# Kernel tuning notes

Hardware: AMD Instinct MI355X
Metric: run time of the kernel (lower is better)

Reference implementation:

```python
import jax, jax.numpy as jnp
import numpy as np

N, IN_DIM, LAT, K = 32768, 128, 64, 8192
BETA = 1.25


def _linear_params(key, d_in, d_out):
    kw, kb = jax.random.split(key)
    lim = 1.0 / np.sqrt(d_in)
    W = jax.random.uniform(kw, (d_out, d_in), minval=-lim, maxval=lim, dtype=jnp.float32)
    b = jax.random.uniform(kb, (d_out,), minval=-lim, maxval=lim, dtype=jnp.float32)
    return W, b


def setup_inputs() -> dict:
    key = jax.random.key(0)
    ks = jax.random.split(key, 9)
    x = jax.random.normal(ks[0], (N, IN_DIM), dtype=jnp.float32)
    # encoder: 128 -> 256 -> 128 -> 64
    enc_W1, enc_b1 = _linear_params(ks[1], IN_DIM, 256)
    enc_W2, enc_b2 = _linear_params(ks[2], 256, 128)
    enc_W3, enc_b3 = _linear_params(ks[3], 128, LAT)
    # codebook: uniform(-1/K, 1/K)
    emb = jax.random.uniform(ks[4], (K, LAT), minval=-1.0 / K, maxval=1.0 / K, dtype=jnp.float32)
    # decoder: 64 -> 128 -> 256 -> (mu: 128, log_var: 128)
    dec_W1, dec_b1 = _linear_params(ks[5], LAT, 128)
    dec_W2, dec_b2 = _linear_params(ks[6], 128, 256)
    dec_Wmu, dec_bmu = _linear_params(ks[7], 256, IN_DIM)
    dec_Wlv, dec_blv = _linear_params(ks[8], 256, IN_DIM)
    return {
        'x': x,
        'enc_W1': enc_W1, 'enc_b1': enc_b1,
        'enc_W2': enc_W2, 'enc_b2': enc_b2,
        'enc_W3': enc_W3, 'enc_b3': enc_b3,
        'emb': emb,
        'dec_W1': dec_W1, 'dec_b1': dec_b1,
        'dec_W2': dec_W2, 'dec_b2': dec_b2,
        'dec_Wmu': dec_Wmu, 'dec_bmu': dec_bmu,
        'dec_Wlv': dec_Wlv, 'dec_blv': dec_blv,
    }


def reference(x, enc_W1, enc_b1, enc_W2, enc_b2, enc_W3, enc_b3, emb,
              dec_W1, dec_b1, dec_W2, dec_b2, dec_Wmu, dec_bmu, dec_Wlv, dec_blv):
    sg = jax.lax.stop_gradient
    # encoder MLP
    h = jax.nn.relu(x @ enc_W1.T + enc_b1)
    h = jax.nn.relu(h @ enc_W2.T + enc_b2)
    lat = h @ enc_W3.T + enc_b3                      # [N, D]
    # vector quantizer: [N, K] pairwise squared distances
    d = (jnp.sum(lat * lat, axis=1, keepdims=True)
         + jnp.sum(emb * emb, axis=1)
         - 2.0 * lat @ emb.T)
    inds = jnp.argmin(d, axis=1)                     # [N]
    one_hot = jax.nn.one_hot(inds, K, dtype=jnp.float32)   # [N, K]
    q = emb[inds]                                    # gather == one_hot @ emb
    commitment = jnp.mean((sg(q) - lat) ** 2)
    embedding_loss = jnp.mean((q - sg(lat)) ** 2)
    vq_loss = BETA * commitment + embedding_loss
    z = lat + sg(q - lat)                            # straight-through
    # decoder MLP
    h = jax.nn.relu(z @ dec_W1.T + dec_b1)
    h = jax.nn.relu(h @ dec_W2.T + dec_b2)
    x_hat = h @ dec_Wmu.T + dec_bmu
    x_hat_var = h @ dec_Wlv.T + dec_blv
    return x_hat, x_hat_var, one_hot, vq_loss
```

## Files before the change

### kernel.cpp

```cpp
#include <hip/hip_runtime.h>
#include <cfloat>
#include <climits>

#define TPB 256


__global__ __launch_bounds__(TPB) void wt_kernel(
    const float* __restrict__ W1, const float* __restrict__ W2,
    const float* __restrict__ W3, const float* __restrict__ U1,
    const float* __restrict__ U2, const float* __restrict__ Umu,
    const float* __restrict__ Ulv, float* __restrict__ wt) {
  __shared__ float sB[64 * 68];
  const int b = blockIdx.x;
  const float* src; int R, C, lt; float* dst;
  if (b < 8)       { src = W1;  R = 256; C = 128; dst = wt;          lt = b; }
  else if (b < 16) { src = W2;  R = 128; C = 256; dst = wt + 32768;  lt = b - 8; }
  else if (b < 18) { src = W3;  R = 64;  C = 128; dst = wt + 65536;  lt = b - 16; }
  else if (b < 20) { src = U1;  R = 128; C = 64;  dst = wt + 73728;  lt = b - 18; }
  else if (b < 28) { src = U2;  R = 256; C = 128; dst = wt + 81920;  lt = b - 20; }
  else if (b < 36) { src = Umu; R = 128; C = 256; dst = wt + 114688; lt = b - 28; }
  else             { src = Ulv; R = 128; C = 256; dst = wt + 147456; lt = b - 36; }
  const int tiles_r = R >> 6;
  const int r0 = (lt % tiles_r) << 6, c0 = (lt / tiles_r) << 6;
  const int t = threadIdx.x;
  for (int v = t; v < 1024; v += TPB) {
    const int c4 = v & 15, r = v >> 4;
    const float4 w =
        *reinterpret_cast<const float4*>(src + (size_t)(r0 + r) * C + c0 + 4 * c4);
    *reinterpret_cast<float4*>(&sB[r * 68 + 4 * c4]) = w;
  }
  __syncthreads();
  for (int v = t; v < 1024; v += TPB) {
    const int r4 = v & 15, c = v >> 4;
    float4 o;
    o.x = sB[(4 * r4 + 0) * 68 + c];
    o.y = sB[(4 * r4 + 1) * 68 + c];
    o.z = sB[(4 * r4 + 2) * 68 + c];
    o.w = sB[(4 * r4 + 3) * 68 + c];
    *reinterpret_cast<float4*>(dst + (size_t)(c0 + c) * R + r0 + 4 * r4) = o;
  }
}

__global__ __launch_bounds__(TPB) void embt_kernel(const float* __restrict__ emb,
                                                   float* __restrict__ embT,
                                                   float* __restrict__ En) {
  __shared__ float sB[64 * 68];
  const int c0 = blockIdx.x * 64;
  const int t = threadIdx.x;
  for (int v = t; v < 1024; v += TPB) {
    const int d4 = v & 15, r = v >> 4;
    const float4 e =
        *reinterpret_cast<const float4*>(emb + (size_t)(c0 + r) * 64 + 4 * d4);
    *reinterpret_cast<float4*>(&sB[r * 68 + 4 * d4]) = e;
  }
  __syncthreads();
  if (t < 64) {
    const float* row = &sB[t * 68];
    float q[8];
#pragma unroll
    for (int j = 0; j < 8; ++j) q[j] = __fmul_rn(row[j], row[j]);
#pragma unroll
    for (int m = 1; m < 8; ++m)
#pragma unroll
      for (int j = 0; j < 8; ++j) {
        const float v = row[m * 8 + j];
        q[j] = __fadd_rn(q[j], __fmul_rn(v, v));
      }
    En[c0 + t] = __fadd_rn(
        __fadd_rn(__fadd_rn(q[0], q[1]), __fadd_rn(q[2], q[3])),
        __fadd_rn(__fadd_rn(q[4], q[5]), __fadd_rn(q[6], q[7])));
  }
  for (int v = t; v < 1024; v += TPB) {
    const int r4 = v & 15, d = v >> 4;
    float4 o;
    o.x = sB[(4 * r4 + 0) * 68 + d];
    o.y = sB[(4 * r4 + 1) * 68 + d];
    o.z = sB[(4 * r4 + 2) * 68 + d];
    o.w = sB[(4 * r4 + 3) * 68 + d];
    *reinterpret_cast<float4*>(embT + (size_t)d * 8192 + c0 + 4 * r4) = o;
  }
}

__global__ __launch_bounds__(512) void enc_fused(
    const float* __restrict__ x, const float* __restrict__ WT1,
    const float* __restrict__ WT2, const float* __restrict__ WT3,
    const float* __restrict__ b1, const float* __restrict__ b2,
    const float* __restrict__ b3, float* __restrict__ lat) {
  __shared__ float sX[128 * 68];
  __shared__ float sH1[256 * 68];
  __shared__ float sH2[128 * 68];
  const int t = threadIdx.x;
  const int m0 = blockIdx.x * 64;

  for (int v = t; v < 2048; v += 512) {
    const int k4 = v & 31, r = v >> 5;
    const float4 xv =
        *reinterpret_cast<const float4*>(x + (size_t)(m0 + r) * 128 + 4 * k4);
    float* dst = &sX[(4 * k4) * 68 + r];
    dst[0] = xv.x; dst[68] = xv.y; dst[136] = xv.z; dst[204] = xv.w;
  }
  __syncthreads();

  {
    const int cg8 = (t & 31) * 8, rg4 = (t >> 5) * 4;
    float acc[4][8] = {};
#pragma unroll 8
    for (int k = 0; k < 128; ++k) {
      const float4 a = *reinterpret_cast<const float4*>(&sX[k * 68 + rg4]);
      const float* wr = WT1 + (size_t)k * 256 + cg8;
      const float4 b0 = *reinterpret_cast<const float4*>(wr);
      const float4 b1v = *reinterpret_cast<const float4*>(wr + 4);
      const float av[4] = {a.x, a.y, a.z, a.w};
      const float bv[8] = {b0.x, b0.y, b0.z, b0.w, b1v.x, b1v.y, b1v.z, b1v.w};
#pragma unroll
      for (int i = 0; i < 4; ++i)
#pragma unroll
        for (int j = 0; j < 8; ++j) acc[i][j] = fmaf(av[i], bv[j], acc[i][j]);
    }
#pragma unroll
    for (int j = 0; j < 8; ++j) {
      const int col = cg8 + j;
      const float bj = b1[col];
#pragma unroll
      for (int i = 0; i < 4; ++i) {
        const float h = __fadd_rn(acc[i][j], bj);
        sH1[col * 68 + rg4 + i] = h > 0.f ? h : 0.f;
      }
    }
  }
  __syncthreads();

  {
    const int cg4 = (t & 31) * 4, rg4 = (t >> 5) * 4;
    float acc[4][4] = {};
#pragma unroll 8
    for (int k = 0; k < 256; ++k) {
      const float4 a = *reinterpret_cast<const float4*>(&sH1[k * 68 + rg4]);
      const float4 bb =
          *reinterpret_cast<const float4*>(WT2 + (size_t)k * 128 + cg4);
      const float av[4] = {a.x, a.y, a.z, a.w};
      const float bv[4] = {bb.x, bb.y, bb.z, bb.w};
#pragma unroll
      for (int i = 0; i < 4; ++i)
#pragma unroll
        for (int j = 0; j < 4; ++j) acc[i][j] = fmaf(av[i], bv[j], acc[i][j]);
    }
#pragma unroll
    for (int j = 0; j < 4; ++j) {
      const int col = cg4 + j;
      const float bj = b2[col];
#pragma unroll
      for (int i = 0; i < 4; ++i) {
        const float h = __fadd_rn(acc[i][j], bj);
        sH2[col * 68 + rg4 + i] = h > 0.f ? h : 0.f;
      }
    }
  }
  __syncthreads();

  {
    const int cg4 = (t & 15) * 4, rg2 = (t >> 4) * 2;
    float acc[2][4] = {};
#pragma unroll 8
    for (int k = 0; k < 128; ++k) {
      const float2 a = *reinterpret_cast<const float2*>(&sH2[k * 68 + rg2]);
      const float4 bb =
          *reinterpret_cast<const float4*>(WT3 + (size_t)k * 64 + cg4);
      const float av[2] = {a.x, a.y};
      const float bv[4] = {bb.x, bb.y, bb.z, bb.w};
#pragma unroll
      for (int i = 0; i < 2; ++i)
#pragma unroll
        for (int j = 0; j < 4; ++j) acc[i][j] = fmaf(av[i], bv[j], acc[i][j]);
    }
#pragma unroll
    for (int i = 0; i < 2; ++i) {
      float4 o;
      o.x = __fadd_rn(acc[i][0], b3[cg4 + 0]);
      o.y = __fadd_rn(acc[i][1], b3[cg4 + 1]);
      o.z = __fadd_rn(acc[i][2], b3[cg4 + 2]);
      o.w = __fadd_rn(acc[i][3], b3[cg4 + 3]);
      *reinterpret_cast<float4*>(lat + (size_t)(m0 + rg2 + i) * 64 + cg4) = o;
    }
  }
}

__global__ __launch_bounds__(512, 6) void vq_kernel(
    const float* __restrict__ lat, const float* __restrict__ embT,
    const float* __restrict__ En, int* __restrict__ inds,
    float* __restrict__ lossp, float* __restrict__ oh) {
  __shared__ float sL[64 * 68];
  __shared__ float sE[64 * 132];
  __shared__ float sEn[128];
  __shared__ float snl[64];
  __shared__ int ridx[64];
  __shared__ float lacc;
  const int t = threadIdx.x;
  const int tx = t & 31, ty = t >> 5;
  const int r0 = ty * 4;
  const int tx4 = tx * 4;
  const int m0 = blockIdx.x * 64;

  for (int v = t; v < 1024; v += 512) {
    const int r = v >> 4, d4 = v & 15;
    const float4 lv =
        *reinterpret_cast<const float4*>(lat + (size_t)(m0 + r) * 64 + 4 * d4);
    float* dst = &sL[(4 * d4) * 68 + r];
    dst[0] = lv.x; dst[68] = lv.y; dst[136] = lv.z; dst[204] = lv.w;
  }
  if (t == 0) lacc = 0.f;
  __syncthreads();
  if (t < 64) {
    float q[8];
#pragma unroll
    for (int j = 0; j < 8; ++j) {
      const float v = sL[j * 68 + t];
      q[j] = __fmul_rn(v, v);
    }
#pragma unroll
    for (int m = 1; m < 8; ++m)
#pragma unroll
      for (int j = 0; j < 8; ++j) {
        const float v = sL[(m * 8 + j) * 68 + t];
        q[j] = __fadd_rn(q[j], __fmul_rn(v, v));
      }
    snl[t] = __fadd_rn(
        __fadd_rn(__fadd_rn(q[0], q[1]), __fadd_rn(q[2], q[3])),
        __fadd_rn(__fadd_rn(q[4], q[5]), __fadd_rn(q[6], q[7])));
  }
  __syncthreads();
  float nl[4];
#pragma unroll
  for (int i = 0; i < 4; ++i) nl[i] = snl[r0 + i];

  float v1[4];
  int i1[4];
#pragma unroll
  for (int i = 0; i < 4; ++i) { v1[i] = FLT_MAX; i1[i] = INT_MAX; }

  for (int ch = 0; ch < 64; ++ch) {
    const int c0 = ch * 128;
    __syncthreads();
    for (int v = t; v < 2048; v += 512) {
      const int cl = v & 31, d = v >> 5;
      const float4 e = *reinterpret_cast<const float4*>(
          embT + (size_t)d * 8192 + c0 + 4 * cl);
      *reinterpret_cast<float4*>(&sE[d * 132 + 4 * cl]) = e;
    }
    if (t < 128) sEn[t] = En[c0 + t];
    __syncthreads();

    float acc[4][4] = {};
#pragma unroll 4
    for (int d = 0; d < 64; ++d) {
      const float4 a = *reinterpret_cast<const float4*>(&sL[d * 68 + r0]);
      const float4 bb = *reinterpret_cast<const float4*>(&sE[d * 132 + tx4]);
      const float av[4] = {a.x, a.y, a.z, a.w};
      const float bv[4] = {bb.x, bb.y, bb.z, bb.w};
#pragma unroll
      for (int i = 0; i < 4; ++i)
#pragma unroll
        for (int j = 0; j < 4; ++j) acc[i][j] = fmaf(av[i], bv[j], acc[i][j]);
    }
#pragma unroll
    for (int j = 0; j < 4; ++j) {
      const float Ec = sEn[tx4 + j];
      const int c = c0 + tx4 + j;
#pragma unroll
      for (int i = 0; i < 4; ++i) {
        const float t1 = __fadd_rn(nl[i], Ec);
        const float s = __fsub_rn(t1, __fmul_rn(2.0f, acc[i][j]));
        if (s < v1[i]) { v1[i] = s; i1[i] = c; }
      }
    }
    const float4 z = make_float4(0.f, 0.f, 0.f, 0.f);
    for (int v = t; v < 2048; v += 512) {
      const int r = v >> 5, c4 = v & 31;
      *reinterpret_cast<float4*>(oh + (size_t)(m0 + r) * 8192 + c0 + 4 * c4) =
          z;
    }
  }

#pragma unroll
  for (int m = 16; m >= 1; m >>= 1) {
#pragma unroll
    for (int i = 0; i < 4; ++i) {
      const float ov = __shfl_xor(v1[i], m);
      const int oi = __shfl_xor(i1[i], m);
      if (ov < v1[i] || (ov == v1[i] && oi < i1[i])) {
        v1[i] = ov; i1[i] = oi;
      }
    }
  }
  if (tx == 0) {
    float ls = 0.f;
#pragma unroll
    for (int i = 0; i < 4; ++i) {
      ridx[r0 + i] = i1[i];
      inds[m0 + r0 + i] = i1[i];
      ls += v1[i];
    }
    atomicAdd(&lacc, ls);
  }
  __syncthreads();
  if (t == 0) lossp[blockIdx.x] = lacc;

  for (int v = t; v < 2048; v += 512) {
    const int r = v >> 5, c4 = v & 31;
    const int ind = ridx[r];
    const int g4 = ind >> 2;
    if ((g4 & 31) == c4) {
      float4 o = make_float4(0.f, 0.f, 0.f, 0.f);
      reinterpret_cast<float*>(&o)[ind & 3] = 1.f;
      *reinterpret_cast<float4*>(oh + (size_t)(m0 + r) * 8192 + 4 * g4) = o;
    }
  }
}

__global__ __launch_bounds__(512) void dec_fused(
    const float* __restrict__ emb, const int* __restrict__ inds,
    const float* __restrict__ WT1, const float* __restrict__ b1,
    const float* __restrict__ WT2, const float* __restrict__ b2,
    const float* __restrict__ WTmu, const float* __restrict__ bmu,
    const float* __restrict__ WTlv, const float* __restrict__ blv,
    float* __restrict__ xh, float* __restrict__ xv) {
  __shared__ float sQ[64 * 68];
  __shared__ float sG1[128 * 68];
  __shared__ float sG2[256 * 68];
  const int t = threadIdx.x;
  const int m0 = blockIdx.x * 64;

  for (int v = t; v < 1024; v += 512) {
    const int k4 = v & 15, r = v >> 4;
    const int id = inds[m0 + r];
    const float4 e =
        *reinterpret_cast<const float4*>(emb + (size_t)id * 64 + 4 * k4);
    float* dst = &sQ[(4 * k4) * 68 + r];
    dst[0] = e.x; dst[68] = e.y; dst[136] = e.z; dst[204] = e.w;
  }
  __syncthreads();

  {
    const int cg4 = (t & 31) * 4, rg4 = (t >> 5) * 4;
    float acc[4][4] = {};
#pragma unroll 8
    for (int k = 0; k < 64; ++k) {
      const float4 a = *reinterpret_cast<const float4*>(&sQ[k * 68 + rg4]);
      const float4 bb =
          *reinterpret_cast<const float4*>(WT1 + (size_t)k * 128 + cg4);
      const float av[4] = {a.x, a.y, a.z, a.w};
      const float bv[4] = {bb.x, bb.y, bb.z, bb.w};
#pragma unroll
      for (int i = 0; i < 4; ++i)
#pragma unroll
        for (int j = 0; j < 4; ++j) acc[i][j] = fmaf(av[i], bv[j], acc[i][j]);
    }
#pragma unroll
    for (int j = 0; j < 4; ++j) {
      const int col = cg4 + j;
      const float bj = b1[col];
#pragma unroll
      for (int i = 0; i < 4; ++i) {
        const float h = acc[i][j] + bj;
        sG1[col * 68 + rg4 + i] = h > 0.f ? h : 0.f;
      }
    }
  }
  __syncthreads();

  {
    const int cg8 = (t & 31) * 8, rg4 = (t >> 5) * 4;
    float acc[4][8] = {};
#pragma unroll 8
    for (int k = 0; k < 128; ++k) {
      const float4 a = *reinterpret_cast<const float4*>(&sG1[k * 68 + rg4]);
      const float* wr = WT2 + (size_t)k * 256 + cg8;
      const float4 b0 = *reinterpret_cast<const float4*>(wr);
      const float4 b1v = *reinterpret_cast<const float4*>(wr + 4);
      const float av[4] = {a.x, a.y, a.z, a.w};
      const float bv[8] = {b0.x, b0.y, b0.z, b0.w, b1v.x, b1v.y, b1v.z, b1v.w};
#pragma unroll
      for (int i = 0; i < 4; ++i)
#pragma unroll
        for (int j = 0; j < 8; ++j) acc[i][j] = fmaf(av[i], bv[j], acc[i][j]);
    }
#pragma unroll
    for (int j = 0; j < 8; ++j) {
      const int col = cg8 + j;
      const float bj = b2[col];
#pragma unroll
      for (int i = 0; i < 4; ++i) {
        const float h = acc[i][j] + bj;
        sG2[col * 68 + rg4 + i] = h > 0.f ? h : 0.f;
      }
    }
  }
  __syncthreads();

  for (int head = 0; head < 2; ++head) {
    const float* WT = head ? WTlv : WTmu;
    const float* bb_ = head ? blv : bmu;
    float* o = head ? xv : xh;
    const int cg4 = (t & 31) * 4, rg4 = (t >> 5) * 4;
    float acc[4][4] = {};
#pragma unroll 8
    for (int k = 0; k < 256; ++k) {
      const float4 a = *reinterpret_cast<const float4*>(&sG2[k * 68 + rg4]);
      const float4 bb =
          *reinterpret_cast<const float4*>(WT + (size_t)k * 128 + cg4);
      const float av[4] = {a.x, a.y, a.z, a.w};
      const float bv[4] = {bb.x, bb.y, bb.z, bb.w};
#pragma unroll
      for (int i = 0; i < 4; ++i)
#pragma unroll
        for (int j = 0; j < 4; ++j) acc[i][j] = fmaf(av[i], bv[j], acc[i][j]);
    }
#pragma unroll
    for (int i = 0; i < 4; ++i) {
      float4 ov;
      ov.x = acc[i][0] + bb_[cg4 + 0];
      ov.y = acc[i][1] + bb_[cg4 + 1];
      ov.z = acc[i][2] + bb_[cg4 + 2];
      ov.w = acc[i][3] + bb_[cg4 + 3];
      *reinterpret_cast<float4*>(o + (size_t)(m0 + rg4 + i) * 128 + cg4) = ov;
    }
  }
}

__global__ void fin_kernel(const float* __restrict__ lossp,
                           float* __restrict__ outp) {
  const int t = threadIdx.x;
  double s = 0.0;
  for (int i = t; i < 512; i += 64) s += (double)lossp[i];
#pragma unroll
  for (int m = 32; m >= 1; m >>= 1) s += __shfl_xor(s, m);
  if (t == 0) *outp = (float)(2.25 * s / (32768.0 * 64.0));
}

extern "C" void kernel_launch(void* const* d_in, const int* in_sizes, int n_in,
                              void* d_out, int out_size, void* d_ws,
                              size_t ws_size, hipStream_t stream) {
  const float* x = (const float*)d_in[0];
  const float* eW1 = (const float*)d_in[1];
  const float* eb1 = (const float*)d_in[2];
  const float* eW2 = (const float*)d_in[3];
  const float* eb2 = (const float*)d_in[4];
  const float* eW3 = (const float*)d_in[5];
  const float* eb3 = (const float*)d_in[6];
  const float* emb = (const float*)d_in[7];
  const float* dW1 = (const float*)d_in[8];
  const float* db1 = (const float*)d_in[9];
  const float* dW2 = (const float*)d_in[10];
  const float* db2 = (const float*)d_in[11];
  const float* dWmu = (const float*)d_in[12];
  const float* dbmu = (const float*)d_in[13];
  const float* dWlv = (const float*)d_in[14];
  const float* dblv = (const float*)d_in[15];

  float* out = (float*)d_out;
  float* xhat = out;
  float* xvar = out + 4194304;
  float* oh = out + 8388608;
  float* lossout = out + 276824064;

  float* lat = (float*)d_ws;
  float* En = lat + 2097152;
  float* lossp = En + 8192;
  int* inds = (int*)(lossp + 512);
  float* embT = (float*)(inds + 32768);
  float* wt = embT + 524288;
  float* wt1 = wt;
  float* wt2 = wt + 32768;
  float* wt3 = wt + 65536;
  float* uwt1 = wt + 73728;
  float* uwt2 = wt + 81920;
  float* uwtmu = wt + 114688;
  float* uwtlv = wt + 147456;

  wt_kernel<<<44, TPB, 0, stream>>>(eW1, eW2, eW3, dW1, dW2, dWmu, dWlv, wt);
  embt_kernel<<<128, TPB, 0, stream>>>(emb, embT, En);
  enc_fused<<<512, 512, 0, stream>>>(x, wt1, wt2, wt3, eb1, eb2, eb3, lat);
  vq_kernel<<<512, 512, 0, stream>>>(lat, embT, En, inds, lossp, oh);
  dec_fused<<<512, 512, 0, stream>>>(emb, inds, uwt1, db1, uwt2, db2, uwtmu,
                                     dbmu, uwtlv, dblv, xhat, xvar);
  fin_kernel<<<1, 64, 0, stream>>>(lossp, lossout);
}
```

Measured before the change: 824.7 us.

## Enlarge VQ distance tile to 128x256 with 8x8 register blocking and prefetch

The VQ kernel now handles 128 rows per block against 256-code chunks, and each thread computes an 8x8 accumulator tile instead of 4x4. This raises arithmetic intensity per shared-memory load and halves the number of code-chunk iterations. The next codebook chunk is prefetched into registers while the current one is being computed, then written to LDS between barriers. The grid halves to 256 blocks and occupancy drops (launch bounds 512,2), with larger LDS use and register pressure. On a 256-CU part this may leave some CUs idle.

New measurement: 834.5 us. Within noise of the previous version (+1.2%).

```diff
diff --git a/kernel.cpp b/kernel.cpp
--- a/kernel.cpp
+++ b/kernel.cpp
@@ -185,43 +185,48 @@
   }
 }
 
-__global__ __launch_bounds__(512, 6) void vq_kernel(
+__global__ __launch_bounds__(512, 2) void vq_kernel(
     const float* __restrict__ lat, const float* __restrict__ embT,
     const float* __restrict__ En, int* __restrict__ inds,
     float* __restrict__ lossp, float* __restrict__ oh) {
-  __shared__ float sL[64 * 68];
-  __shared__ float sE[64 * 132];
-  __shared__ float sEn[128];
-  __shared__ float snl[64];
-  __shared__ int ridx[64];
+  __shared__ float sL[64 * 132];
+  __shared__ float sE[64 * 260];
+  __shared__ float snl[128];
+  __shared__ int ridx[128];
   __shared__ float lacc;
   const int t = threadIdx.x;
-  const int tx = t & 31, ty = t >> 5;
-  const int r0 = ty * 4;
-  const int tx4 = tx * 4;
-  const int m0 = blockIdx.x * 64;
-
-  for (int v = t; v < 1024; v += 512) {
+  const int cg = t & 31;
+  const int rg = t >> 5;
+  const int cg4 = cg * 4;
+  const int rg4 = rg * 4;
+  const int m0 = blockIdx.x * 128;
+
+  for (int v = t; v < 2048; v += 512) {
     const int r = v >> 4, d4 = v & 15;
     const float4 lv =
         *reinterpret_cast<const float4*>(lat + (size_t)(m0 + r) * 64 + 4 * d4);
-    float* dst = &sL[(4 * d4) * 68 + r];
-    dst[0] = lv.x; dst[68] = lv.y; dst[136] = lv.z; dst[204] = lv.w;
+    float* dst = &sL[(4 * d4) * 132 + r];
+    dst[0] = lv.x; dst[132] = lv.y; dst[264] = lv.z; dst[396] = lv.w;
+  }
+  for (int v = t; v < 4096; v += 512) {
+    const int d = v >> 6, c4 = v & 63;
+    *reinterpret_cast<float4*>(&sE[d * 260 + 4 * c4]) =
+        *reinterpret_cast<const float4*>(embT + (size_t)d * 8192 + 4 * c4);
   }
   if (t == 0) lacc = 0.f;
   __syncthreads();
-  if (t < 64) {
+  if (t < 128) {
     float q[8];
 #pragma unroll
     for (int j = 0; j < 8; ++j) {
-      const float v = sL[j * 68 + t];
+      const float v = sL[j * 132 + t];
       q[j] = __fmul_rn(v, v);
     }
 #pragma unroll
     for (int m = 1; m < 8; ++m)
 #pragma unroll
       for (int j = 0; j < 8; ++j) {
-        const float v = sL[(m * 8 + j) * 68 + t];
+        const float v = sL[(m * 8 + j) * 132 + t];
         q[j] = __fadd_rn(q[j], __fmul_rn(v, v));
       }
     snl[t] = __fadd_rn(
@@ -229,62 +234,87 @@
         __fadd_rn(__fadd_rn(q[4], q[5]), __fadd_rn(q[6], q[7])));
   }
   __syncthreads();
-  float nl[4];
-#pragma unroll
-  for (int i = 0; i < 4; ++i) nl[i] = snl[r0 + i];
-
-  float v1[4];
-  int i1[4];
-#pragma unroll
-  for (int i = 0; i < 4; ++i) { v1[i] = FLT_MAX; i1[i] = INT_MAX; }
-
-  for (int ch = 0; ch < 64; ++ch) {
-    const int c0 = ch * 128;
-    __syncthreads();
-    for (int v = t; v < 2048; v += 512) {
-      const int cl = v & 31, d = v >> 5;
-      const float4 e = *reinterpret_cast<const float4*>(
-          embT + (size_t)d * 8192 + c0 + 4 * cl);
-      *reinterpret_cast<float4*>(&sE[d * 132 + 4 * cl]) = e;
-    }
-    if (t < 128) sEn[t] = En[c0 + t];
-    __syncthreads();
-
-    float acc[4][4] = {};
-#pragma unroll 4
+  float nl[8];
+#pragma unroll
+  for (int i = 0; i < 4; ++i) {
+    nl[i] = snl[rg4 + i];
+    nl[4 + i] = snl[64 + rg4 + i];
+  }
+
+  float v1[8];
+  int i1[8];
+#pragma unroll
+  for (int i = 0; i < 8; ++i) { v1[i] = FLT_MAX; i1[i] = INT_MAX; }
+
+  const float4 z = make_float4(0.f, 0.f, 0.f, 0.f);
+
+  for (int ch = 0; ch < 32; ++ch) {
+    const int c0 = ch << 8;
+    float4 pf[8];
+    if (ch < 31) {
+      const int cn = c0 + 256;
+#pragma unroll
+      for (int k = 0; k < 8; ++k) {
+        const int v = t + (k << 9);
+        const int d = v >> 6, c4 = v & 63;
+        pf[k] = *reinterpret_cast<const float4*>(embT + (size_t)d * 8192 +
+                                                 cn + 4 * c4);
+      }
+    }
+    const float4 EA = *reinterpret_cast<const float4*>(En + c0 + cg4);
+    const float4 EB = *reinterpret_cast<const float4*>(En + c0 + 128 + cg4);
+
+    float acc[8][8] = {};
+#pragma unroll 2
     for (int d = 0; d < 64; ++d) {
-      const float4 a = *reinterpret_cast<const float4*>(&sL[d * 68 + r0]);
-      const float4 bb = *reinterpret_cast<const float4*>(&sE[d * 132 + tx4]);
-      const float av[4] = {a.x, a.y, a.z, a.w};
-      const float bv[4] = {bb.x, bb.y, bb.z, bb.w};
-#pragma unroll
-      for (int i = 0; i < 4; ++i)
-#pragma unroll
-        for (int j = 0; j < 4; ++j) acc[i][j] = fmaf(av[i], bv[j], acc[i][j]);
-    }
-#pragma unroll
-    for (int j = 0; j < 4; ++j) {
-      const float Ec = sEn[tx4 + j];
-      const int c = c0 + tx4 + j;
-#pragma unroll
-      for (int i = 0; i < 4; ++i) {
+      const float4 a0 = *reinterpret_cast<const float4*>(&sL[d * 132 + rg4]);
+      const float4 a1 =
+          *reinterpret_cast<const float4*>(&sL[d * 132 + 64 + rg4]);
+      const float4 b0 = *reinterpret_cast<const float4*>(&sE[d * 260 + cg4]);
+      const float4 b1 =
+          *reinterpret_cast<const float4*>(&sE[d * 260 + 128 + cg4]);
+      const float av[8] = {a0.x, a0.y, a0.z, a0.w, a1.x, a1.y, a1.z, a1.w};
+      const float bv[8] = {b0.x, b0.y, b0.z, b0.w, b1.x, b1.y, b1.z, b1.w};
+#pragma unroll
+      for (int i = 0; i < 8; ++i)
+#pragma unroll
+        for (int j = 0; j < 8; ++j) acc[i][j] = fmaf(av[i], bv[j], acc[i][j]);
+    }
+    const float Ev[8] = {EA.x, EA.y, EA.z, EA.w, EB.x, EB.y, EB.z, EB.w};
+#pragma unroll
+    for (int j = 0; j < 8; ++j) {
+      const int c = c0 + (j < 4 ? cg4 + j : 128 + cg4 + (j - 4));
+      const float Ec = Ev[j];
+#pragma unroll
+      for (int i = 0; i < 8; ++i) {
         const float t1 = __fadd_rn(nl[i], Ec);
         const float s = __fsub_rn(t1, __fmul_rn(2.0f, acc[i][j]));
         if (s < v1[i]) { v1[i] = s; i1[i] = c; }
       }
     }
-    const float4 z = make_float4(0.f, 0.f, 0.f, 0.f);
-    for (int v = t; v < 2048; v += 512) {
-      const int r = v >> 5, c4 = v & 31;
+#pragma unroll
+    for (int k = 0; k < 16; ++k) {
+      const int v = t + (k << 9);
+      const int r = v >> 6, c4 = v & 63;
       *reinterpret_cast<float4*>(oh + (size_t)(m0 + r) * 8192 + c0 + 4 * c4) =
           z;
     }
+    __syncthreads();
+    if (ch < 31) {
+#pragma unroll
+      for (int k = 0; k < 8; ++k) {
+        const int v = t + (k << 9);
+        const int d = v >> 6, c4 = v & 63;
+        *reinterpret_cast<float4*>(&sE[d * 260 + 4 * c4]) = pf[k];
+      }
+    }
+    __syncthreads();
   }
 
 #pragma unroll
   for (int m = 16; m >= 1; m >>= 1) {
 #pragma unroll
-    for (int i = 0; i < 4; ++i) {
+    for (int i = 0; i < 8; ++i) {
       const float ov = __shfl_xor(v1[i], m);
       const int oi = __shfl_xor(i1[i], m);
       if (ov < v1[i] || (ov == v1[i] && oi < i1[i])) {
@@ -292,24 +322,29 @@
       }
     }
   }
-  if (tx == 0) {
+  if (cg == 0) {
     float ls = 0.f;
 #pragma unroll
     for (int i = 0; i < 4; ++i) {
-      ridx[r0 + i] = i1[i];
-      inds[m0 + r0 + i] = i1[i];
+      ridx[rg4 + i] = i1[i];
+      inds[m0 + rg4 + i] = i1[i];
       ls += v1[i];
+      ridx[64 + rg4 + i] = i1[4 + i];
+      inds[m0 + 64 + rg4 + i] = i1[4 + i];
+      ls += v1[4 + i];
     }
     atomicAdd(&lacc, ls);
   }
   __syncthreads();
   if (t == 0) lossp[blockIdx.x] = lacc;
 
-  for (int v = t; v < 2048; v += 512) {
-    const int r = v >> 5, c4 = v & 31;
+#pragma unroll
+  for (int k = 0; k < 16; ++k) {
+    const int v = t + (k << 9);
+    const int r = v >> 6, c4 = v & 63;
     const int ind = ridx[r];
     const int g4 = ind >> 2;
-    if ((g4 & 31) == c4) {
+    if ((g4 & 63) == c4) {
       float4 o = make_float4(0.f, 0.f, 0.f, 0.f);
       reinterpret_cast<float*>(&o)[ind & 3] = 1.f;
       *reinterpret_cast<float4*>(oh + (size_t)(m0 + r) * 8192 + 4 * g4) = o;
@@ -431,7 +466,7 @@
                            float* __restrict__ outp) {
   const int t = threadIdx.x;
   double s = 0.0;
-  for (int i = t; i < 512; i += 64) s += (double)lossp[i];
+  for (int i = t; i < 256; i += 64) s += (double)lossp[i];
 #pragma unroll
   for (int m = 32; m >= 1; m >>= 1) s += __shfl_xor(s, m);
   if (t == 0) *outp = (float)(2.25 * s / (32768.0 * 64.0));
@@ -480,7 +515,7 @@
   wt_kernel<<<44, TPB, 0, stream>>>(eW1, eW2, eW3, dW1, dW2, dWmu, dWlv, wt);
   embt_kernel<<<128, TPB, 0, stream>>>(emb, embT, En);
   enc_fused<<<512, 512, 0, stream>>>(x, wt1, wt2, wt3, eb1, eb2, eb3, lat);
-  vq_kernel<<<512, 512, 0, stream>>>(lat, embT, En, inds, lossp, oh);
+  vq_kernel<<<256, 512, 0, stream>>>(lat, embT, En, inds, lossp, oh);
   dec_fused<<<512, 512, 0, stream>>>(emb, inds, uwt1, db1, uwt2, db2, uwtmu,
                                      dbmu, uwtlv, dblv, xhat, xvar);
   fin_kernel<<<1, 64, 0, stream>>>(lossp, lossout);
```

## Fuse VQ search and decoder into one kernel with prefetch and nontemporal stores

Applied to the files above, without the earlier changes.

Merges the vector-quantizer kernel and the decoder MLP into a single kernel, so the chosen indices stay in shared memory and the separate inds global round trip and one launch go away. The codebook chunk for the next iteration is prefetched into registers while the current chunk is processed. The large one-hot zero fill and the decoder outputs now use nontemporal stores. The decoder's 256-wide hidden layer is split into two 128-column halves so one shared buffer can be reused, which cuts shared memory, and the occupancy hint is lowered from 6 to 4 blocks.

New measurement: 833.0 us. About the same (+1.0%).

```diff
diff --git a/kernel.cpp b/kernel.cpp
--- a/kernel.cpp
+++ b/kernel.cpp
@@ -4,6 +4,14 @@
 
 #define TPB 256
 
+
+typedef float f32x4 __attribute__((ext_vector_type(4)));
+
+__device__ __forceinline__ void nt_store4(float* p, float4 v) {
+  f32x4 nv;
+  nv.x = v.x; nv.y = v.y; nv.z = v.z; nv.w = v.w;
+  __builtin_nontemporal_store(nv, reinterpret_cast<f32x4*>(p));
+}
 
 __global__ __launch_bounds__(TPB) void wt_kernel(
     const float* __restrict__ W1, const float* __restrict__ W2,
@@ -185,244 +193,308 @@
   }
 }
 
-__global__ __launch_bounds__(512, 6) void vq_kernel(
+__global__ __launch_bounds__(512, 4) void vqdec_kernel(
     const float* __restrict__ lat, const float* __restrict__ embT,
-    const float* __restrict__ En, int* __restrict__ inds,
-    float* __restrict__ lossp, float* __restrict__ oh) {
-  __shared__ float sL[64 * 68];
-  __shared__ float sE[64 * 132];
-  __shared__ float sEn[128];
+    const float* __restrict__ En, const float* __restrict__ emb,
+    const float* __restrict__ UT1, const float* __restrict__ ub1,
+    const float* __restrict__ UT2, const float* __restrict__ ub2,
+    const float* __restrict__ UTmu, const float* __restrict__ ubmu,
+    const float* __restrict__ UTlv, const float* __restrict__ ublv,
+    float* __restrict__ oh, float* __restrict__ xh, float* __restrict__ xv,
+    float* __restrict__ lossp) {
+  __shared__ float smem[13056];
   __shared__ float snl[64];
   __shared__ int ridx[64];
   __shared__ float lacc;
   const int t = threadIdx.x;
-  const int tx = t & 31, ty = t >> 5;
-  const int r0 = ty * 4;
-  const int tx4 = tx * 4;
   const int m0 = blockIdx.x * 64;
 
-  for (int v = t; v < 1024; v += 512) {
-    const int r = v >> 4, d4 = v & 15;
-    const float4 lv =
-        *reinterpret_cast<const float4*>(lat + (size_t)(m0 + r) * 64 + 4 * d4);
-    float* dst = &sL[(4 * d4) * 68 + r];
-    dst[0] = lv.x; dst[68] = lv.y; dst[136] = lv.z; dst[204] = lv.w;
-  }
-  if (t == 0) lacc = 0.f;
-  __syncthreads();
-  if (t < 64) {
-    float q[8];
-#pragma unroll
-    for (int j = 0; j < 8; ++j) {
-      const float v = sL[j * 68 + t];
-      q[j] = __fmul_rn(v, v);
-    }
-#pragma unroll
-    for (int m = 1; m < 8; ++m)
+  {
+    float* const sL = smem;
+    float* const sE = smem + 4352;
+    const int cg = t & 31, rg = t >> 5;
+    const int cg4 = cg * 4, rg4 = rg * 4;
+
+    for (int v = t; v < 1024; v += 512) {
+      const int r = v >> 4, d4 = v & 15;
+      const float4 lv =
+          *reinterpret_cast<const float4*>(lat + (size_t)(m0 + r) * 64 + 4 * d4);
+      float* dst = &sL[(4 * d4) * 68 + r];
+      dst[0] = lv.x; dst[68] = lv.y; dst[136] = lv.z; dst[204] = lv.w;
+    }
+    if (t == 0) lacc = 0.f;
+    float4 st[4];
+#pragma unroll
+    for (int k = 0; k < 4; ++k) {
+      const int v = t + (k << 9);
+      const int d = v >> 5, c4 = v & 31;
+      st[k] = *reinterpret_cast<const float4*>(embT + (size_t)d * 8192 + 4 * c4);
+    }
+    __syncthreads();
+    if (t < 64) {
+      float q[8];
 #pragma unroll
       for (int j = 0; j < 8; ++j) {
-        const float v = sL[(m * 8 + j) * 68 + t];
-        q[j] = __fadd_rn(q[j], __fmul_rn(v, v));
-      }
-    snl[t] = __fadd_rn(
-        __fadd_rn(__fadd_rn(q[0], q[1]), __fadd_rn(q[2], q[3])),
-        __fadd_rn(__fadd_rn(q[4], q[5]), __fadd_rn(q[6], q[7])));
-  }
-  __syncthreads();
-  float nl[4];
-#pragma unroll
-  for (int i = 0; i < 4; ++i) nl[i] = snl[r0 + i];
-
-  float v1[4];
-  int i1[4];
-#pragma unroll
-  for (int i = 0; i < 4; ++i) { v1[i] = FLT_MAX; i1[i] = INT_MAX; }
-
-  for (int ch = 0; ch < 64; ++ch) {
-    const int c0 = ch * 128;
-    __syncthreads();
-    for (int v = t; v < 2048; v += 512) {
-      const int cl = v & 31, d = v >> 5;
-      const float4 e = *reinterpret_cast<const float4*>(
-          embT + (size_t)d * 8192 + c0 + 4 * cl);
-      *reinterpret_cast<float4*>(&sE[d * 132 + 4 * cl]) = e;
-    }
-    if (t < 128) sEn[t] = En[c0 + t];
-    __syncthreads();
-
-    float acc[4][4] = {};
+        const float v = sL[j * 68 + t];
+        q[j] = __fmul_rn(v, v);
+      }
+#pragma unroll
+      for (int m = 1; m < 8; ++m)
+#pragma unroll
+        for (int j = 0; j < 8; ++j) {
+          const float v = sL[(m * 8 + j) * 68 + t];
+          q[j] = __fadd_rn(q[j], __fmul_rn(v, v));
+        }
+      snl[t] = __fadd_rn(
+          __fadd_rn(__fadd_rn(q[0], q[1]), __fadd_rn(q[2], q[3])),
+          __fadd_rn(__fadd_rn(q[4], q[5]), __fadd_rn(q[6], q[7])));
+    }
+    __syncthreads();
+    float nl[4];
+#pragma unroll
+    for (int i = 0; i < 4; ++i) nl[i] = snl[rg4 + i];
+
+    float v1[4];
+    int i1[4];
+#pragma unroll
+    for (int i = 0; i < 4; ++i) { v1[i] = FLT_MAX; i1[i] = INT_MAX; }
+
+    const float4 z = make_float4(0.f, 0.f, 0.f, 0.f);
+
+    for (int ch = 0; ch < 64; ++ch) {
+      const int c0 = ch << 7;
+#pragma unroll
+      for (int k = 0; k < 4; ++k) {
+        const int v = t + (k << 9);
+        const int d = v >> 5, c4 = v & 31;
+        *reinterpret_cast<float4*>(&sE[d * 132 + 4 * c4]) = st[k];
+      }
+      __syncthreads();
+#pragma unroll
+      for (int k = 0; k < 4; ++k) {
+        const int v = t + (k << 9);
+        const int r = v >> 5, c4 = v & 31;
+        nt_store4(oh + (size_t)(m0 + r) * 8192 + c0 + 4 * c4, z);
+      }
+      if (ch < 63) {
+        const int cn = c0 + 128;
+#pragma unroll
+        for (int k = 0; k < 4; ++k) {
+          const int v = t + (k << 9);
+          const int d = v >> 5, c4 = v & 31;
+          st[k] = *reinterpret_cast<const float4*>(embT + (size_t)d * 8192 +
+                                                   cn + 4 * c4);
+        }
+      }
+      const float4 EA = *reinterpret_cast<const float4*>(En + c0 + cg4);
+
+      float acc[4][4] = {};
 #pragma unroll 4
-    for (int d = 0; d < 64; ++d) {
-      const float4 a = *reinterpret_cast<const float4*>(&sL[d * 68 + r0]);
-      const float4 bb = *reinterpret_cast<const float4*>(&sE[d * 132 + tx4]);
+      for (int d = 0; d < 64; ++d) {
+        const float4 a = *reinterpret_cast<const float4*>(&sL[d * 68 + rg4]);
+        const float4 bb = *reinterpret_cast<const float4*>(&sE[d * 132 + cg4]);
+        const float av[4] = {a.x, a.y, a.z, a.w};
+        const float bv[4] = {bb.x, bb.y, bb.z, bb.w};
+#pragma unroll
+        for (int i = 0; i < 4; ++i)
+#pragma unroll
+          for (int j = 0; j < 4; ++j) acc[i][j] = fmaf(av[i], bv[j], acc[i][j]);
+      }
+      const float Ev[4] = {EA.x, EA.y, EA.z, EA.w};
+#pragma unroll
+      for (int j = 0; j < 4; ++j) {
+        const int c = c0 + cg4 + j;
+        const float Ec = Ev[j];
+#pragma unroll
+        for (int i = 0; i < 4; ++i) {
+          const float t1 = __fadd_rn(nl[i], Ec);
+          const float s = __fsub_rn(t1, __fmul_rn(2.0f, acc[i][j]));
+          if (s < v1[i]) { v1[i] = s; i1[i] = c; }
+        }
+      }
+      __syncthreads();
+    }
+
+#pragma unroll
+    for (int m = 16; m >= 1; m >>= 1) {
+#pragma unroll
+      for (int i = 0; i < 4; ++i) {
+        const float ov = __shfl_xor(v1[i], m);
+        const int oi = __shfl_xor(i1[i], m);
+        if (ov < v1[i] || (ov == v1[i] && oi < i1[i])) {
+          v1[i] = ov; i1[i] = oi;
+        }
+      }
+    }
+    if (cg == 0) {
+      float ls = 0.f;
+#pragma unroll
+      for (int i = 0; i < 4; ++i) {
+        ridx[rg4 + i] = i1[i];
+        ls += v1[i];
+      }
+      atomicAdd(&lacc, ls);
+    }
+    __syncthreads();
+    if (t == 0) lossp[blockIdx.x] = lacc;
+
+#pragma unroll
+    for (int k = 0; k < 4; ++k) {
+      const int v = t + (k << 9);
+      const int r = v >> 5, c4 = v & 31;
+      const int ind = ridx[r];
+      const int g4 = ind >> 2;
+      if ((g4 & 31) == c4) {
+        float4 o = make_float4(0.f, 0.f, 0.f, 0.f);
+        reinterpret_cast<float*>(&o)[ind & 3] = 1.f;
+        nt_store4(oh + (size_t)(m0 + r) * 8192 + 4 * g4, o);
+      }
+    }
+  }
+
+  {
+    float* const sQ = smem;
+    float* const sG1 = smem + 4352;
+    float* const sG2 = smem;
+
+    for (int v = t; v < 1024; v += 512) {
+      const int k4 = v & 15, r = v >> 4;
+      const int id = ridx[r];
+      const float4 e =
+          *reinterpret_cast<const float4*>(emb + (size_t)id * 64 + 4 * k4);
+      float* dst = &sQ[(4 * k4) * 68 + r];
+      dst[0] = e.x; dst[68] = e.y; dst[136] = e.z; dst[204] = e.w;
+    }
+    __syncthreads();
+
+    const int cg4 = (t & 31) * 4, rg4 = (t >> 5) * 4;
+
+    {
+      float acc[4][4] = {};
+#pragma unroll 8
+      for (int k = 0; k < 64; ++k) {
+        const float4 a = *reinterpret_cast<const float4*>(&sQ[k * 68 + rg4]);
+        const float4 bb =
+            *reinterpret_cast<const float4*>(UT1 + (size_t)k * 128 + cg4);
+        const float av[4] = {a.x, a.y, a.z, a.w};
+        const float bv[4] = {bb.x, bb.y, bb.z, bb.w};
+#pragma unroll
+        for (int i = 0; i < 4; ++i)
+#pragma unroll
+          for (int j = 0; j < 4; ++j) acc[i][j] = fmaf(av[i], bv[j], acc[i][j]);
+      }
+#pragma unroll
+      for (int j = 0; j < 4; ++j) {
+        const int col = cg4 + j;
+        const float bj = ub1[col];
+#pragma unroll
+        for (int i = 0; i < 4; ++i) {
+          const float h = acc[i][j] + bj;
+          sG1[col * 68 + rg4 + i] = h > 0.f ? h : 0.f;
+        }
+      }
+    }
+    __syncthreads();
+
+    float accA[4][4] = {}, accB[4][4] = {};
+#pragma unroll 8
+    for (int k = 0; k < 128; ++k) {
+      const float4 a = *reinterpret_cast<const float4*>(&sG1[k * 68 + rg4]);
+      const float4 bA =
+          *reinterpret_cast<const float4*>(UT2 + (size_t)k * 256 + cg4);
+      const float4 bB =
+          *reinterpret_cast<const float4*>(UT2 + (size_t)k * 256 + 128 + cg4);
       const float av[4] = {a.x, a.y, a.z, a.w};
-      const float bv[4] = {bb.x, bb.y, bb.z, bb.w};
+      const float bAv[4] = {bA.x, bA.y, bA.z, bA.w};
+      const float bBv[4] = {bB.x, bB.y, bB.z, bB.w};
 #pragma unroll
       for (int i = 0; i < 4; ++i)
 #pragma unroll
-        for (int j = 0; j < 4; ++j) acc[i][j] = fmaf(av[i], bv[j], acc[i][j]);
-    }
-#pragma unroll
-    for (int j = 0; j < 4; ++j) {
-      const float Ec = sEn[tx4 + j];
-      const int c = c0 + tx4 + j;
-#pragma unroll
-      for (int i = 0; i < 4; ++i) {
-        const float t1 = __fadd_rn(nl[i], Ec);
-        const float s = __fsub_rn(t1, __fmul_rn(2.0f, acc[i][j]));
-        if (s < v1[i]) { v1[i] = s; i1[i] = c; }
-      }
-    }
-    const float4 z = make_float4(0.f, 0.f, 0.f, 0.f);
-    for (int v = t; v < 2048; v += 512) {
-      const int r = v >> 5, c4 = v & 31;
-      *reinterpret_cast<float4*>(oh + (size_t)(m0 + r) * 8192 + c0 + 4 * c4) =
-          z;
-    }
-  }
-
-#pragma unroll
-  for (int m = 16; m >= 1; m >>= 1) {
-#pragma unroll
-    for (int i = 0; i < 4; ++i) {
-      const float ov = __shfl_xor(v1[i], m);
-      const int oi = __shfl_xor(i1[i], m);
-      if (ov < v1[i] || (ov == v1[i] && oi < i1[i])) {
-        v1[i] = ov; i1[i] = oi;
-      }
-    }
-  }
-  if (tx == 0) {
-    float ls = 0.f;
-#pragma unroll
-    for (int i = 0; i < 4; ++i) {
-      ridx[r0 + i] = i1[i];
-      inds[m0 + r0 + i] = i1[i];
-      ls += v1[i];
-    }
-    atomicAdd(&lacc, ls);
-  }
-  __syncthreads();
-  if (t == 0) lossp[blockIdx.x] = lacc;
-
-  for (int v = t; v < 2048; v += 512) {
-    const int r = v >> 5, c4 = v & 31;
-    const int ind = ridx[r];
-    const int g4 = ind >> 2;
-    if ((g4 & 31) == c4) {
-      float4 o = make_float4(0.f, 0.f, 0.f, 0.f);
-      reinterpret_cast<float*>(&o)[ind & 3] = 1.f;
-      *reinterpret_cast<float4*>(oh + (size_t)(m0 + r) * 8192 + 4 * g4) = o;
-    }
-  }
-}
-
-__global__ __launch_bounds__(512) void dec_fused(
-    const float* __restrict__ emb, const int* __restrict__ inds,
-    const float* __restrict__ WT1, const float* __restrict__ b1,
-    const float* __restrict__ WT2, const float* __restrict__ b2,
-    const float* __restrict__ WTmu, const float* __restrict__ bmu,
-    const float* __restrict__ WTlv, const float* __restrict__ blv,
-    float* __restrict__ xh, float* __restrict__ xv) {
-  __shared__ float sQ[64 * 68];
-  __shared__ float sG1[128 * 68];
-  __shared__ float sG2[256 * 68];
-  const int t = threadIdx.x;
-  const int m0 = blockIdx.x * 64;
-
-  for (int v = t; v < 1024; v += 512) {
-    const int k4 = v & 15, r = v >> 4;
-    const int id = inds[m0 + r];
-    const float4 e =
-        *reinterpret_cast<const float4*>(emb + (size_t)id * 64 + 4 * k4);
-    float* dst = &sQ[(4 * k4) * 68 + r];
-    dst[0] = e.x; dst[68] = e.y; dst[136] = e.z; dst[204] = e.w;
-  }
-  __syncthreads();
-
-  {
-    const int cg4 = (t & 31) * 4, rg4 = (t >> 5) * 4;
-    float acc[4][4] = {};
-#pragma unroll 8
-    for (int k = 0; k < 64; ++k) {
-      const float4 a = *reinterpret_cast<const float4*>(&sQ[k * 68 + rg4]);
-      const float4 bb =
-          *reinterpret_cast<const float4*>(WT1 + (size_t)k * 128 + cg4);
-      const float av[4] = {a.x, a.y, a.z, a.w};
-      const float bv[4] = {bb.x, bb.y, bb.z, bb.w};
-#pragma unroll
-      for (int i = 0; i < 4; ++i)
-#pragma unroll
-        for (int j = 0; j < 4; ++j) acc[i][j] = fmaf(av[i], bv[j], acc[i][j]);
-    }
+        for (int j = 0; j < 4; ++j) {
+          accA[i][j] = fmaf(av[i], bAv[j], accA[i][j]);
+          accB[i][j] = fmaf(av[i], bBv[j], accB[i][j]);
+        }
+    }
+    __syncthreads();
+
 #pragma unroll
     for (int j = 0; j < 4; ++j) {
       const int col = cg4 + j;
-      const float bj = b1[col];
+      const float bj = ub2[col];
 #pragma unroll
       for (int i = 0; i < 4; ++i) {
-        const float h = acc[i][j] + bj;
-        sG1[col * 68 + rg4 + i] = h > 0.f ? h : 0.f;
-      }
-    }
-  }
-  __syncthreads();
-
-  {
-    const int cg8 = (t & 31) * 8, rg4 = (t >> 5) * 4;
-    float acc[4][8] = {};
-#pragma unroll 8
-    for (int k = 0; k < 128; ++k) {
-      const float4 a = *reinterpret_cast<const float4*>(&sG1[k * 68 + rg4]);
-      const float* wr = WT2 + (size_t)k * 256 + cg8;
-      const float4 b0 = *reinterpret_cast<const float4*>(wr);
-      const float4 b1v = *reinterpret_cast<const float4*>(wr + 4);
+        const float h = accA[i][j] + bj;
+        sG2[col * 68 + rg4 + i] = h > 0.f ? h : 0.f;
+      }
+    }
+    __syncthreads();
+
+    float accH[2][4][4] = {};
+#pragma unroll 8
+    for (int c = 0; c < 128; ++c) {
+      const float4 a = *reinterpret_cast<const float4*>(&sG2[c * 68 + rg4]);
+      const float4 bm =
+          *reinterpret_cast<const float4*>(UTmu + (size_t)c * 128 + cg4);
+      const float4 bl =
+          *reinterpret_cast<const float4*>(UTlv + (size_t)c * 128 + cg4);
       const float av[4] = {a.x, a.y, a.z, a.w};
-      const float bv[8] = {b0.x, b0.y, b0.z, b0.w, b1v.x, b1v.y, b1v.z, b1v.w};
+      const float bmv[4] = {bm.x, bm.y, bm.z, bm.w};
+      const float blv_[4] = {bl.x, bl.y, bl.z, bl.w};
 #pragma unroll
       for (int i = 0; i < 4; ++i)
 #pragma unroll
-        for (int j = 0; j < 8; ++j) acc[i][j] = fmaf(av[i], bv[j], acc[i][j]);
-    }
-#pragma unroll
-    for (int j = 0; j < 8; ++j) {
-      const int col = cg8 + j;
-      const float bj = b2[col];
+        for (int j = 0; j < 4; ++j) {
+          accH[0][i][j] = fmaf(av[i], bmv[j], accH[0][i][j]);
+          accH[1][i][j] = fmaf(av[i], blv_[j], accH[1][i][j]);
+        }
+    }
+    __syncthreads();
+
+#pragma unroll
+    for (int j = 0; j < 4; ++j) {
+      const int col = 128 + cg4 + j;
+      const float bj = ub2[col];
 #pragma unroll
       for (int i = 0; i < 4; ++i) {
-        const float h = acc[i][j] + bj;
-        sG2[col * 68 + rg4 + i] = h > 0.f ? h : 0.f;
-      }
-    }
-  }
-  __syncthreads();
-
-  for (int head = 0; head < 2; ++head) {
-    const float* WT = head ? WTlv : WTmu;
-    const float* bb_ = head ? blv : bmu;
-    float* o = head ? xv : xh;
-    const int cg4 = (t & 31) * 4, rg4 = (t >> 5) * 4;
-    float acc[4][4] = {};
-#pragma unroll 8
-    for (int k = 0; k < 256; ++k) {
-      const float4 a = *reinterpret_cast<const float4*>(&sG2[k * 68 + rg4]);
-      const float4 bb =
-          *reinterpret_cast<const float4*>(WT + (size_t)k * 128 + cg4);
+        const float h = accB[i][j] + bj;
+        sG2[(cg4 + j) * 68 + rg4 + i] = h > 0.f ? h : 0.f;
+      }
+    }
+    __syncthreads();
+
+#pragma unroll 8
+    for (int c = 0; c < 128; ++c) {
+      const float4 a = *reinterpret_cast<const float4*>(&sG2[c * 68 + rg4]);
+      const float4 bm = *reinterpret_cast<const float4*>(
+          UTmu + (size_t)(128 + c) * 128 + cg4);
+      const float4 bl = *reinterpret_cast<const float4*>(
+          UTlv + (size_t)(128 + c) * 128 + cg4);
       const float av[4] = {a.x, a.y, a.z, a.w};
-      const float bv[4] = {bb.x, bb.y, bb.z, bb.w};
+      const float bmv[4] = {bm.x, bm.y, bm.z, bm.w};
+      const float blv_[4] = {bl.x, bl.y, bl.z, bl.w};
 #pragma unroll
       for (int i = 0; i < 4; ++i)
 #pragma unroll
-        for (int j = 0; j < 4; ++j) acc[i][j] = fmaf(av[i], bv[j], acc[i][j]);
-    }
+        for (int j = 0; j < 4; ++j) {
+          accH[0][i][j] = fmaf(av[i], bmv[j], accH[0][i][j]);
+          accH[1][i][j] = fmaf(av[i], blv_[j], accH[1][i][j]);
+        }
+    }
+
 #pragma unroll
     for (int i = 0; i < 4; ++i) {
       float4 ov;
-      ov.x = acc[i][0] + bb_[cg4 + 0];
-      ov.y = acc[i][1] + bb_[cg4 + 1];
-      ov.z = acc[i][2] + bb_[cg4 + 2];
-      ov.w = acc[i][3] + bb_[cg4 + 3];
-      *reinterpret_cast<float4*>(o + (size_t)(m0 + rg4 + i) * 128 + cg4) = ov;
+      ov.x = accH[0][i][0] + ubmu[cg4 + 0];
+      ov.y = accH[0][i][1] + ubmu[cg4 + 1];
+      ov.z = accH[0][i][2] + ubmu[cg4 + 2];
+      ov.w = accH[0][i][3] + ubmu[cg4 + 3];
+      nt_store4(xh + (size_t)(m0 + rg4 + i) * 128 + cg4, ov);
+      float4 ov2;
+      ov2.x = accH[1][i][0] + ublv[cg4 + 0];
+      ov2.y = accH[1][i][1] + ublv[cg4 + 1];
+      ov2.z = accH[1][i][2] + ublv[cg4 + 2];
+      ov2.w = accH[1][i][3] + ublv[cg4 + 3];
+      nt_store4(xv + (size_t)(m0 + rg4 + i) * 128 + cg4, ov2);
     }
   }
 }
@@ -480,8 +552,8 @@
   wt_kernel<<<44, TPB, 0, stream>>>(eW1, eW2, eW3, dW1, dW2, dWmu, dWlv, wt);
   embt_kernel<<<128, TPB, 0, stream>>>(emb, embT, En);
   enc_fused<<<512, 512, 0, stream>>>(x, wt1, wt2, wt3, eb1, eb2, eb3, lat);
-  vq_kernel<<<512, 512, 0, stream>>>(lat, embT, En, inds, lossp, oh);
-  dec_fused<<<512, 512, 0, stream>>>(emb, inds, uwt1, db1, uwt2, db2, uwtmu,
-                                     dbmu, uwtlv, dblv, xhat, xvar);
+  vqdec_kernel<<<512, 512, 0, stream>>>(lat, embT, En, emb, uwt1, db1, uwt2,
+                                        db2, uwtmu, dbmu, uwtlv, dblv, oh,
+                                        xhat, xvar, lossp);
   fin_kernel<<<1, 64, 0, stream>>>(lossp, lossout);
 }
```
